# Kernel optimization log

Hardware: AMD Instinct MI355X
Metric: run time of the kernel (lower is better)

The kernel has to match this reference:

```python
import jax, jax.numpy as jnp
import numpy as np

B, E, G, D, L = 16384, 2048, 32, 128, 2  # batch, len_embeddings, b_matrices, d_mid_cols, num_hidden_layers
LN_EPS = 1e-3  # keras LayerNormalization default epsilon


def _make_indices():
    # generate_structured_indices_uniformly_ with seed_offset = layer_id*1000 = 0
    idx = np.zeros((G, D), dtype=np.int32)
    for i in range(G):
        rng = np.random.RandomState(i)
        idx[i] = rng.permutation(E)[:D]
    return jnp.asarray(idx)


def setup_inputs() -> dict:
    key = jax.random.key(0)
    kx, kw, kb = jax.random.split(key, 3)
    x = jax.random.normal(kx, (B, E), dtype=jnp.float32)
    W = jax.random.normal(kw, (G, L, D, D), dtype=jnp.float32) * (1.0 / np.sqrt(D))
    b = jax.random.normal(kb, (G, L, D), dtype=jnp.float32) * 0.02
    gamma = jnp.ones((G, D), dtype=jnp.float32)
    beta = jnp.zeros((G, D), dtype=jnp.float32)
    return {"x": x, "indices": _make_indices(), "W": W, "b": b,
            "gamma": gamma, "beta": beta}


def reference(x, indices, W, b, gamma, beta):
    # Fixed-index gather: [B, E] -> [B, G, D]
    g = jnp.take(x, indices, axis=1)
    h = g
    # Per-block Dense+GELU stack, batched over blocks as a grouped GEMM
    n_layers = W.shape[1]
    for l in range(n_layers):
        h = jax.nn.gelu(jnp.einsum('bgd,gde->bge', h, W[:, l]) + b[:, l][None],
                        approximate=False)
    # Residual + per-block LayerNorm over last axis
    h = h + g
    mu = jnp.mean(h, axis=-1, keepdims=True)
    var = jnp.mean(jnp.square(h - mu), axis=-1, keepdims=True)
    out = (h - mu) * jax.lax.rsqrt(var + LN_EPS) * gamma[None] + beta[None]
    return out  # [B, G, D]
```

## Files before the change

### kernel.cpp

```cpp
#include <hip/hip_runtime.h>
#include <math.h>
#include <stdint.h>


constexpr int E_DIM = 2048;
constexpr int G_DIM = 32;
constexpr int D_DIM = 128;
constexpr float LN_EPS = 1e-3f;

constexpr int ROWS1 = 4;
constexpr int BM    = 128;
constexpr int AW    = 136;

typedef float f32x4  __attribute__((ext_vector_type(4)));
typedef short bf16x8 __attribute__((ext_vector_type(8)));

__device__ __forceinline__ short f2bf(float f) {
    uint32_t u = __builtin_bit_cast(uint32_t, f);
    uint32_t r = (u + 0x7fffu + ((u >> 16) & 1u)) >> 16;
    return (short)r;
}
__device__ __forceinline__ float bf2f(short s) {
    uint32_t u = ((uint32_t)(uint16_t)s) << 16;
    return __builtin_bit_cast(float, u);
}
__device__ __forceinline__ float gelu_fast(float x) {
    const float x2 = x * x;
    const float z  = 2.30220817f * x * fmaf(0.044715f, x2, 1.0f);
    const float e  = __builtin_amdgcn_exp2f(-z);
    return x * __builtin_amdgcn_rcpf(1.0f + e);
}

__global__ __launch_bounds__(256) void ssb_wprep_kernel(
    const float* __restrict__ W, short* __restrict__ Wf)
{
    const int t    = blockIdx.x * 256 + threadIdx.x;
    const int lane = t & 63;
    const int ks   = (t >> 6) & 3;
    const int nt   = (t >> 8) & 7;
    const int gl   = t >> 11;
    const float* Wl = W + (size_t)gl * D_DIM * D_DIM;
    const int n  = nt * 16 + (lane & 15);
    const int k0 = ks * 32 + ((lane >> 4) << 3);
    short* dst = Wf + (size_t)t * 8;
    #pragma unroll
    for (int j = 0; j < 8; ++j) dst[j] = f2bf(Wl[(size_t)(k0 + j) * D_DIM + n]);
}

template<bool WS>
__global__ __launch_bounds__(256) void ssb_gather_kernel(
    const float* __restrict__ x,
    const int*   __restrict__ idx,
    float* __restrict__ outF,
    short* __restrict__ outH)
{
    __shared__ float sX[ROWS1][E_DIM];
    __shared__ int   sIdx[G_DIM * D_DIM];

    const int tid  = threadIdx.x;
    const int row0 = blockIdx.x * ROWS1;

    for (int i = tid; i < G_DIM * D_DIM; i += 256) sIdx[i] = idx[i];

    #pragma unroll
    for (int r = 0; r < ROWS1; ++r) {
        const float4* src = (const float4*)(x + (size_t)(row0 + r) * E_DIM);
        float4* dst = (float4*)sX[r];
        dst[tid]       = src[tid];
        dst[tid + 256] = src[tid + 256];
    }
    __syncthreads();

    #pragma unroll
    for (int r = 0; r < ROWS1; ++r) {
        const size_t base = (size_t)(row0 + r) * G_DIM * D_DIM;
        #pragma unroll
        for (int t = 0; t < 4; ++t) {
            const int j = (t * 256 + tid) * 4;
            const float v0 = sX[r][sIdx[j]],     v1 = sX[r][sIdx[j + 1]];
            const float v2 = sX[r][sIdx[j + 2]], v3 = sX[r][sIdx[j + 3]];
            if (WS) {
                short4 v; v.x = f2bf(v0); v.y = f2bf(v1); v.z = f2bf(v2); v.w = f2bf(v3);
                *(short4*)(outH + base + j) = v;
            } else {
                *(float4*)(outF + base + j) = make_float4(v0, v1, v2, v3);
            }
        }
    }
}

template<bool WS>
__global__ __launch_bounds__(256, 4) void ssb_mfma_kernel(
    const short* __restrict__ Wf,
    const short* __restrict__ actH,
    const float* __restrict__ bias,
    const float* __restrict__ gamma,
    const float* __restrict__ beta,
    float* __restrict__ out)
{
    __shared__ __align__(16) short sAct[4][32 * AW];

    const int g    = blockIdx.y;
    const int tid  = threadIdx.x;
    const int lane = tid & 63;
    const int wv   = tid >> 6;
    const int q    = lane >> 4;
    const int c16  = lane & 15;
    const size_t rbase = (size_t)blockIdx.x * BM + wv * 32;

    short* strip = sAct[wv];

    #pragma unroll
    for (int i = 0; i < 8; ++i) {
        const int rl = 8 * q + i;
        const size_t off = ((rbase + rl) * G_DIM + g) * D_DIM + 8 * c16;
        bf16x8 p;
        if (WS) {
            p = *(const bf16x8*)(actH + off);
        } else {
            const float4* src = (const float4*)(out + off);
            const float4 a0 = src[0], a1 = src[1];
            p[0] = f2bf(a0.x); p[1] = f2bf(a0.y); p[2] = f2bf(a0.z); p[3] = f2bf(a0.w);
            p[4] = f2bf(a1.x); p[5] = f2bf(a1.y); p[6] = f2bf(a1.z); p[7] = f2bf(a1.w);
        }
        *(bf16x8*)(strip + rl * AW + 8 * c16) = p;
    }

    const short* Wg0 = Wf + (size_t)(g * 2 + 0) * (D_DIM * D_DIM);
    const short* Wg1 = Wf + (size_t)(g * 2 + 1) * (D_DIM * D_DIM);

    f32x4 acc0[8], acc1[8];

    #pragma unroll
    for (int nt = 0; nt < 8; ++nt) { acc0[nt] = (f32x4){0,0,0,0}; acc1[nt] = (f32x4){0,0,0,0}; }
    #pragma unroll
    for (int ks = 0; ks < 4; ++ks) {
        const bf16x8 a0 = *(const bf16x8*)(strip + (     c16) * AW + ks * 32 + q * 8);
        const bf16x8 a1 = *(const bf16x8*)(strip + (16 + c16) * AW + ks * 32 + q * 8);
        #pragma unroll
        for (int nt = 0; nt < 8; ++nt) {
            const bf16x8 bfr = *(const bf16x8*)(Wg0 + (nt * 4 + ks) * 512 + lane * 8);
            acc0[nt] = __builtin_amdgcn_mfma_f32_16x16x32_bf16(a0, bfr, acc0[nt], 0, 0, 0);
            acc1[nt] = __builtin_amdgcn_mfma_f32_16x16x32_bf16(a1, bfr, acc1[nt], 0, 0, 0);
        }
    }

    {
        const float* bl0 = bias + (g * 2 + 0) * D_DIM;
        #pragma unroll
        for (int nt = 0; nt < 8; ++nt) {
            const float b0 = bl0[nt * 16 + c16];
            #pragma unroll
            for (int j = 0; j < 4; ++j) {
                strip[(     4 * q + j) * AW + nt * 16 + c16] = f2bf(gelu_fast(acc0[nt][j] + b0));
                strip[(16 + 4 * q + j) * AW + nt * 16 + c16] = f2bf(gelu_fast(acc1[nt][j] + b0));
            }
        }
    }

    #pragma unroll
    for (int nt = 0; nt < 8; ++nt) { acc0[nt] = (f32x4){0,0,0,0}; acc1[nt] = (f32x4){0,0,0,0}; }
    #pragma unroll
    for (int ks = 0; ks < 4; ++ks) {
        const bf16x8 a0 = *(const bf16x8*)(strip + (     c16) * AW + ks * 32 + q * 8);
        const bf16x8 a1 = *(const bf16x8*)(strip + (16 + c16) * AW + ks * 32 + q * 8);
        #pragma unroll
        for (int nt = 0; nt < 8; ++nt) {
            const bf16x8 bfr = *(const bf16x8*)(Wg1 + (nt * 4 + ks) * 512 + lane * 8);
            acc0[nt] = __builtin_amdgcn_mfma_f32_16x16x32_bf16(a0, bfr, acc0[nt], 0, 0, 0);
            acc1[nt] = __builtin_amdgcn_mfma_f32_16x16x32_bf16(a1, bfr, acc1[nt], 0, 0, 0);
        }
    }

    const float* bl1 = bias + (g * 2 + 1) * D_DIM;
    float b1[8], gm[8], bt[8];
    #pragma unroll
    for (int nt = 0; nt < 8; ++nt) {
        b1[nt] = bl1[nt * 16 + c16];
        gm[nt] = gamma[g * D_DIM + nt * 16 + c16];
        bt[nt] = beta [g * D_DIM + nt * 16 + c16];
    }

    auto epilogue = [&](const f32x4* acc, int mt) {
        const size_t r0 = (rbase + mt * 16 + 4 * q) * (size_t)(G_DIM * D_DIM) + (size_t)g * D_DIM + c16;
        const short* rp = actH + r0;
        const float* fp = out  + r0;
        float s[4] = {0,0,0,0}, s2[4] = {0,0,0,0};
        #pragma unroll
        for (int j = 0; j < 4; ++j) {
            #pragma unroll
            for (int nt = 0; nt < 8; ++nt) {
                const float res = WS ? bf2f(rp[j * 4096 + nt * 16]) : fp[j * 4096 + nt * 16];
                const float v = gelu_fast(acc[nt][j] + b1[nt]) + res;
                s[j] += v; s2[j] += v * v;
            }
        }
        float mu[4], rs[4];
        #pragma unroll
        for (int j = 0; j < 4; ++j) {
            #pragma unroll
            for (int m = 8; m >= 1; m >>= 1) {
                s[j]  += __shfl_xor(s[j],  m, 64);
                s2[j] += __shfl_xor(s2[j], m, 64);
            }
            mu[j] = s[j] * (1.0f / 128.0f);
            const float var = fmaxf(s2[j] * (1.0f / 128.0f) - mu[j] * mu[j], 0.f);
            rs[j] = rsqrtf(var + LN_EPS);
        }
        float* op = out + r0;
        #pragma unroll
        for (int j = 0; j < 4; ++j) {
            #pragma unroll
            for (int nt = 0; nt < 8; ++nt) {
                const float res = WS ? bf2f(rp[j * 4096 + nt * 16]) : fp[j * 4096 + nt * 16];
                const float v = gelu_fast(acc[nt][j] + b1[nt]) + res;
                op[j * 4096 + nt * 16] = (v - mu[j]) * rs[j] * gm[nt] + bt[nt];
            }
        }
    };
    epilogue(acc0, 0);
    epilogue(acc1, 1);
}

extern "C" void kernel_launch(void* const* d_in, const int* in_sizes, int n_in,
                              void* d_out, int out_size, void* d_ws, size_t ws_size,
                              hipStream_t stream) {
    const float* x     = (const float*)d_in[0];
    const int*   idx   = (const int*)d_in[1];
    const float* W     = (const float*)d_in[2];
    const float* b     = (const float*)d_in[3];
    const float* gamma = (const float*)d_in[4];
    const float* beta  = (const float*)d_in[5];
    float* out = (float*)d_out;
    short* Wf  = (short*)d_ws;

    const int B = in_sizes[0] / E_DIM;
    const size_t wfElems  = (size_t)G_DIM * 2 * D_DIM * D_DIM;
    const size_t actElems = (size_t)B * G_DIM * D_DIM;
    const bool useWs = ws_size >= (wfElems + actElems) * sizeof(short);
    short* actH = Wf + wfElems;

    ssb_wprep_kernel<<<dim3(512), 256, 0, stream>>>(W, Wf);
    if (useWs) {
        ssb_gather_kernel<true ><<<dim3(B / ROWS1), 256, 0, stream>>>(x, idx, out, actH);
        ssb_mfma_kernel <true ><<<dim3(B / BM, G_DIM), 256, 0, stream>>>(Wf, actH, b, gamma, beta, out);
    } else {
        ssb_gather_kernel<false><<<dim3(B / ROWS1), 256, 0, stream>>>(x, idx, out, actH);
        ssb_mfma_kernel <false><<<dim3(B / BM, G_DIM), 256, 0, stream>>>(Wf, actH, b, gamma, beta, out);
    }
}
```

Baseline: 256.5 us.

## Load layer-1 A fragments directly to registers, fold bias into accumulators, cache epilogue values

The gather kernel now keeps its indices in registers loaded straight from global memory instead of staging them in shared memory. The MFMA kernel loads the first layer's A fragments directly from global memory into registers, skipping the LDS store and reload. Biases are used as the initial accumulator value rather than added afterwards. The epilogue stores the GELU+residual value back into the accumulator, so the second pass no longer re-reads the residual or recomputes GELU. This raises register pressure and makes the first-layer global loads less coalesced (16 rows at 16-byte granularity).

Result: slower. 262.4 us (+2.3%).

```diff
diff --git a/kernel.cpp b/kernel.cpp
--- a/kernel.cpp
+++ b/kernel.cpp
@@ -55,12 +55,14 @@
     short* __restrict__ outH)
 {
     __shared__ float sX[ROWS1][E_DIM];
-    __shared__ int   sIdx[G_DIM * D_DIM];
 
     const int tid  = threadIdx.x;
     const int row0 = blockIdx.x * ROWS1;
 
-    for (int i = tid; i < G_DIM * D_DIM; i += 256) sIdx[i] = idx[i];
+    const int4 iv0 = *(const int4*)(idx + (0 * 256 + tid) * 4);
+    const int4 iv1 = *(const int4*)(idx + (1 * 256 + tid) * 4);
+    const int4 iv2 = *(const int4*)(idx + (2 * 256 + tid) * 4);
+    const int4 iv3 = *(const int4*)(idx + (3 * 256 + tid) * 4);
 
     #pragma unroll
     for (int r = 0; r < ROWS1; ++r) {
@@ -76,9 +78,10 @@
         const size_t base = (size_t)(row0 + r) * G_DIM * D_DIM;
         #pragma unroll
         for (int t = 0; t < 4; ++t) {
+            const int4 iv = (t == 0) ? iv0 : (t == 1) ? iv1 : (t == 2) ? iv2 : iv3;
             const int j = (t * 256 + tid) * 4;
-            const float v0 = sX[r][sIdx[j]],     v1 = sX[r][sIdx[j + 1]];
-            const float v2 = sX[r][sIdx[j + 2]], v3 = sX[r][sIdx[j + 3]];
+            const float v0 = sX[r][iv.x], v1 = sX[r][iv.y];
+            const float v2 = sX[r][iv.z], v3 = sX[r][iv.w];
             if (WS) {
                 short4 v; v.x = f2bf(v0); v.y = f2bf(v1); v.z = f2bf(v2); v.w = f2bf(v3);
                 *(short4*)(outH + base + j) = v;
@@ -107,23 +110,32 @@
     const int q    = lane >> 4;
     const int c16  = lane & 15;
     const size_t rbase = (size_t)blockIdx.x * BM + wv * 32;
+    const size_t rowE  = (size_t)G_DIM * D_DIM;
 
     short* strip = sAct[wv];
 
-    #pragma unroll
-    for (int i = 0; i < 8; ++i) {
-        const int rl = 8 * q + i;
-        const size_t off = ((rbase + rl) * G_DIM + g) * D_DIM + 8 * c16;
-        bf16x8 p;
-        if (WS) {
-            p = *(const bf16x8*)(actH + off);
-        } else {
-            const float4* src = (const float4*)(out + off);
-            const float4 a0 = src[0], a1 = src[1];
-            p[0] = f2bf(a0.x); p[1] = f2bf(a0.y); p[2] = f2bf(a0.z); p[3] = f2bf(a0.w);
-            p[4] = f2bf(a1.x); p[5] = f2bf(a1.y); p[6] = f2bf(a1.z); p[7] = f2bf(a1.w);
-        }
-        *(bf16x8*)(strip + rl * AW + 8 * c16) = p;
+    bf16x8 a0f[4], a1f[4];
+    {
+        const size_t base0 = (rbase + c16) * rowE + (size_t)g * D_DIM + q * 8;
+        const size_t base1 = base0 + 16 * rowE;
+        #pragma unroll
+        for (int ks = 0; ks < 4; ++ks) {
+            if (WS) {
+                a0f[ks] = *(const bf16x8*)(actH + base0 + ks * 32);
+                a1f[ks] = *(const bf16x8*)(actH + base1 + ks * 32);
+            } else {
+                const float4 f0 = *(const float4*)(out + base0 + ks * 32);
+                const float4 f1 = *(const float4*)(out + base0 + ks * 32 + 4);
+                const float4 f2 = *(const float4*)(out + base1 + ks * 32);
+                const float4 f3 = *(const float4*)(out + base1 + ks * 32 + 4);
+                bf16x8 p0, p1;
+                p0[0] = f2bf(f0.x); p0[1] = f2bf(f0.y); p0[2] = f2bf(f0.z); p0[3] = f2bf(f0.w);
+                p0[4] = f2bf(f1.x); p0[5] = f2bf(f1.y); p0[6] = f2bf(f1.z); p0[7] = f2bf(f1.w);
+                p1[0] = f2bf(f2.x); p1[1] = f2bf(f2.y); p1[2] = f2bf(f2.z); p1[3] = f2bf(f2.w);
+                p1[4] = f2bf(f3.x); p1[5] = f2bf(f3.y); p1[6] = f2bf(f3.z); p1[7] = f2bf(f3.w);
+                a0f[ks] = p0; a1f[ks] = p1;
+            }
+        }
     }
 
     const short* Wg0 = Wf + (size_t)(g * 2 + 0) * (D_DIM * D_DIM);
@@ -131,67 +143,74 @@
 
     f32x4 acc0[8], acc1[8];
 
-    #pragma unroll
-    for (int nt = 0; nt < 8; ++nt) { acc0[nt] = (f32x4){0,0,0,0}; acc1[nt] = (f32x4){0,0,0,0}; }
+    {
+        const float* bl0 = bias + (g * 2 + 0) * D_DIM;
+        #pragma unroll
+        for (int nt = 0; nt < 8; ++nt) {
+            const float b = bl0[nt * 16 + c16];
+            acc0[nt] = (f32x4){b, b, b, b};
+            acc1[nt] = (f32x4){b, b, b, b};
+        }
+    }
+    #pragma unroll
+    for (int ks = 0; ks < 4; ++ks) {
+        #pragma unroll
+        for (int nt = 0; nt < 8; ++nt) {
+            const bf16x8 bfr = *(const bf16x8*)(Wg0 + (nt * 4 + ks) * 512 + lane * 8);
+            acc0[nt] = __builtin_amdgcn_mfma_f32_16x16x32_bf16(a0f[ks], bfr, acc0[nt], 0, 0, 0);
+            acc1[nt] = __builtin_amdgcn_mfma_f32_16x16x32_bf16(a1f[ks], bfr, acc1[nt], 0, 0, 0);
+        }
+    }
+
+    #pragma unroll
+    for (int nt = 0; nt < 8; ++nt) {
+        #pragma unroll
+        for (int j = 0; j < 4; ++j) {
+            strip[(     4 * q + j) * AW + nt * 16 + c16] = f2bf(gelu_fast(acc0[nt][j]));
+            strip[(16 + 4 * q + j) * AW + nt * 16 + c16] = f2bf(gelu_fast(acc1[nt][j]));
+        }
+    }
+
+    {
+        const float* bl1 = bias + (g * 2 + 1) * D_DIM;
+        #pragma unroll
+        for (int nt = 0; nt < 8; ++nt) {
+            const float b = bl1[nt * 16 + c16];
+            acc0[nt] = (f32x4){b, b, b, b};
+            acc1[nt] = (f32x4){b, b, b, b};
+        }
+    }
     #pragma unroll
     for (int ks = 0; ks < 4; ++ks) {
         const bf16x8 a0 = *(const bf16x8*)(strip + (     c16) * AW + ks * 32 + q * 8);
         const bf16x8 a1 = *(const bf16x8*)(strip + (16 + c16) * AW + ks * 32 + q * 8);
         #pragma unroll
         for (int nt = 0; nt < 8; ++nt) {
-            const bf16x8 bfr = *(const bf16x8*)(Wg0 + (nt * 4 + ks) * 512 + lane * 8);
-            acc0[nt] = __builtin_amdgcn_mfma_f32_16x16x32_bf16(a0, bfr, acc0[nt], 0, 0, 0);
-            acc1[nt] = __builtin_amdgcn_mfma_f32_16x16x32_bf16(a1, bfr, acc1[nt], 0, 0, 0);
-        }
-    }
-
-    {
-        const float* bl0 = bias + (g * 2 + 0) * D_DIM;
-        #pragma unroll
-        for (int nt = 0; nt < 8; ++nt) {
-            const float b0 = bl0[nt * 16 + c16];
-            #pragma unroll
-            for (int j = 0; j < 4; ++j) {
-                strip[(     4 * q + j) * AW + nt * 16 + c16] = f2bf(gelu_fast(acc0[nt][j] + b0));
-                strip[(16 + 4 * q + j) * AW + nt * 16 + c16] = f2bf(gelu_fast(acc1[nt][j] + b0));
-            }
-        }
-    }
-
-    #pragma unroll
-    for (int nt = 0; nt < 8; ++nt) { acc0[nt] = (f32x4){0,0,0,0}; acc1[nt] = (f32x4){0,0,0,0}; }
-    #pragma unroll
-    for (int ks = 0; ks < 4; ++ks) {
-        const bf16x8 a0 = *(const bf16x8*)(strip + (     c16) * AW + ks * 32 + q * 8);
-        const bf16x8 a1 = *(const bf16x8*)(strip + (16 + c16) * AW + ks * 32 + q * 8);
-        #pragma unroll
-        for (int nt = 0; nt < 8; ++nt) {
             const bf16x8 bfr = *(const bf16x8*)(Wg1 + (nt * 4 + ks) * 512 + lane * 8);
             acc0[nt] = __builtin_amdgcn_mfma_f32_16x16x32_bf16(a0, bfr, acc0[nt], 0, 0, 0);
             acc1[nt] = __builtin_amdgcn_mfma_f32_16x16x32_bf16(a1, bfr, acc1[nt], 0, 0, 0);
         }
     }
 
-    const float* bl1 = bias + (g * 2 + 1) * D_DIM;
-    float b1[8], gm[8], bt[8];
+    float gm[8], bt[8];
     #pragma unroll
     for (int nt = 0; nt < 8; ++nt) {
-        b1[nt] = bl1[nt * 16 + c16];
         gm[nt] = gamma[g * D_DIM + nt * 16 + c16];
         bt[nt] = beta [g * D_DIM + nt * 16 + c16];
     }
 
-    auto epilogue = [&](const f32x4* acc, int mt) {
-        const size_t r0 = (rbase + mt * 16 + 4 * q) * (size_t)(G_DIM * D_DIM) + (size_t)g * D_DIM + c16;
+    auto epilogue = [&](f32x4* acc, int mt) {
+        const size_t r0 = (rbase + mt * 16 + 4 * q) * rowE + (size_t)g * D_DIM + c16;
         const short* rp = actH + r0;
         const float* fp = out  + r0;
-        float s[4] = {0,0,0,0}, s2[4] = {0,0,0,0};
+        float s[4] = {0, 0, 0, 0}, s2[4] = {0, 0, 0, 0};
         #pragma unroll
         for (int j = 0; j < 4; ++j) {
             #pragma unroll
             for (int nt = 0; nt < 8; ++nt) {
                 const float res = WS ? bf2f(rp[j * 4096 + nt * 16]) : fp[j * 4096 + nt * 16];
-                const float v = gelu_fast(acc[nt][j] + b1[nt]) + res;
+                const float v = gelu_fast(acc[nt][j]) + res;
+                acc[nt][j] = v;
                 s[j] += v; s2[j] += v * v;
             }
         }
@@ -212,9 +231,7 @@
         for (int j = 0; j < 4; ++j) {
             #pragma unroll
             for (int nt = 0; nt < 8; ++nt) {
-                const float res = WS ? bf2f(rp[j * 4096 + nt * 16]) : fp[j * 4096 + nt * 16];
-                const float v = gelu_fast(acc[nt][j] + b1[nt]) + res;
-                op[j * 4096 + nt * 16] = (v - mu[j]) * rs[j] * gm[nt] + bt[nt];
+                op[j * 4096 + nt * 16] = (acc[nt][j] - mu[j]) * rs[j] * gm[nt] + bt[nt];
             }
         }
     };
```
